# Kernel tuning notes

Measured on AMD Instinct MI355X. Metric: run time of the kernel, lower is better.

## Reference

```python
import jax, jax.numpy as jnp
import numpy as np

EPS = 1e-5
HEADS = 4
DQK = 128
DV = 128
SCALE = DQK ** -0.5


def _bn(x, g, b, m, v):
    # inference-mode BatchNorm over channel dim (axis=1)
    inv = g / jnp.sqrt(v + EPS)
    return x * inv[None, :, None, None] + (b - m * inv)[None, :, None, None]


def setup_inputs() -> dict:
    key = jax.random.key(0)
    ks = jax.random.split(key, 16)
    f = lambda i, shape, s=1.0: jax.random.normal(ks[i], shape, dtype=jnp.float32) * s
    N, Cin, H, W = 16, 2048, 32, 32
    mid = HEADS * DV  # 512
    return {
        "x": f(0, (N, Cin, H, W)),
        "conv1_w": f(1, (mid, Cin), 0.02),
        "gamma1": 1.0 + f(2, (mid,), 0.02),
        "beta1": f(3, (mid,), 0.02),
        "mean1": f(4, (mid,), 0.02),
        "var1": 1.0 + 0.1 * jax.random.uniform(ks[5], (mid,), dtype=jnp.float32),
        "qk_w": f(6, (2 * HEADS * DQK, mid), 0.02),
        "v_w": f(7, (HEADS * DV, mid), 0.02),
        "pos_h": f(8, (H, DQK), SCALE),
        "pos_w": f(9, (W, DQK), SCALE),
        "conv3_w": f(10, (Cin, mid), 0.02),
        "gamma3": 1.0 + f(11, (Cin,), 0.02),
        "beta3": f(12, (Cin,), 0.02),
        "mean3": f(13, (Cin,), 0.02),
        "var3": 1.0 + 0.1 * jax.random.uniform(ks[14], (Cin,), dtype=jnp.float32),
    }


def reference(x, conv1_w, gamma1, beta1, mean1, var1, qk_w, v_w, pos_h, pos_w,
              conv3_w, gamma3, beta3, mean3, var3):
    n, c, h, w = x.shape
    # conv1 (1x1) + BN + ReLU
    out = jnp.einsum('nchw,oc->nohw', x, conv1_w)
    out = jax.nn.relu(_bn(out, gamma1, beta1, mean1, var1))
    # MHSA
    qk = jnp.einsum('nchw,oc->nohw', out, qk_w)  # [n, 2*heads*dqk, h, w]
    vv = jnp.einsum('nchw,oc->nohw', out, v_w)   # [n, heads*dv, h, w]
    q, k = jnp.split(qk, 2, axis=1)

    def to_heads(t):
        d = t.shape[1] // HEADS
        return t.reshape(n, HEADS, d, h * w).transpose(0, 1, 3, 2)  # [n, H, hw, d]

    q, k, vv = to_heads(q), to_heads(k), to_heads(vv)
    q = q * SCALE
    # absolute positional embedding: emb[(h w), d]
    emb = (pos_h[:, None, :] + pos_w[None, :, :]).reshape(h * w, DQK)
    logits = jnp.einsum('nhxd,nhyd->nhxy', q, k) + jnp.einsum('nhxd,yd->nhxy', q, emb)
    weights = jax.nn.softmax(logits, axis=-1)
    attn = jnp.einsum('nhxy,nhyd->nhxd', weights, vv)  # [n, H, hw, dv]
    attn = attn.transpose(0, 1, 3, 2).reshape(n, HEADS * DV, h, w)
    # stride=1 -> avg_pool is identity
    attn = jax.nn.relu(attn)
    # conv3 (1x1) + BN
    out = jnp.einsum('nchw,oc->nohw', attn, conv3_w)
    out = _bn(out, gamma3, beta3, mean3, var3)
    # residual (downsample=None, in==out channels, stride=1) + ReLU
    return jax.nn.relu(out + x)
```

## Files before the change

kernel.cpp:

```cpp
#include <hip/hip_runtime.h>
#include <stdint.h>

typedef __bf16 bf16_t;
typedef __bf16 bf16x8 __attribute__((ext_vector_type(8)));
typedef float f32x4 __attribute__((ext_vector_type(4)));

#define EPSV 1e-5f
#define QSCALE 0.08838834764831845f
#define NB 16
#define HWD 1024
#define CIN 2048
#define MID 512
#define QKLD 1024

__device__ __forceinline__ void gl_lds16(const bf16_t* g, void* l) {
    __builtin_amdgcn_global_load_lds(
        (const __attribute__((address_space(1))) uint32_t*)g,
        (__attribute__((address_space(3))) uint32_t*)l, 16, 0, 0);
}

__device__ __forceinline__ f32x4 mfma16(bf16x8 a, bf16x8 b, f32x4 c) {
    return __builtin_amdgcn_mfma_f32_16x16x32_bf16(a, b, c, 0, 0, 0);
}

#define PW1 (512*2048)
#define PQK (PW1 + 1024*512)
#define PV  (PQK + 512*512)
#define PW3 (PV  + 2048*512)
#define PE  (PW3 + 1024*128)

__global__ void prep_kernel(const float* __restrict__ conv1_w,
                            const float* __restrict__ qk_w,
                            const float* __restrict__ v_w,
                            const float* __restrict__ pos_h,
                            const float* __restrict__ pos_w,
                            const float* __restrict__ conv3_w,
                            bf16_t* __restrict__ w1b, bf16_t* __restrict__ wqkb,
                            bf16_t* __restrict__ wvb, bf16_t* __restrict__ w3b,
                            float* __restrict__ emb) {
    int stride = gridDim.x * blockDim.x;
    for (int i = blockIdx.x * blockDim.x + threadIdx.x; i < PE; i += stride) {
        if (i < PW1) {
            w1b[i] = (bf16_t)conv1_w[i];
        } else if (i < PQK) {
            int j = i - PW1;
            int row = j >> 9;
            float v = (row < 512) ? qk_w[j] * QSCALE : qk_w[j];
            wqkb[j] = (bf16_t)v;
        } else if (i < PV) {
            int j = i - PQK;
            wvb[j] = (bf16_t)v_w[j];
        } else if (i < PW3) {
            int j = i - PV;
            w3b[j] = (bf16_t)conv3_w[j];
        } else {
            int j = i - PW3;
            int y = j >> 7, d = j & 127;
            emb[j] = pos_h[(y >> 5) * 128 + d] + pos_w[(y & 31) * 128 + d];
        }
    }
}

__global__ void transpose_x_kernel(const float* __restrict__ x, bf16_t* __restrict__ xt) {
    __shared__ uint32_t tileT[64][20];
    const int n = blockIdx.z;
    const int c0 = blockIdx.x * 32;
    const int hw0 = blockIdx.y * 64;
    const int t = threadIdx.x;

    const int cp = t >> 4;
    const int hw4 = (t & 15) * 4;
    const float* p0 = x + ((size_t)n * CIN + c0 + 2 * cp) * HWD + hw0 + hw4;
    const float4 a = *(const float4*)p0;
    const float4 b = *(const float4*)(p0 + HWD);
    float av[4] = {a.x, a.y, a.z, a.w};
    float bv[4] = {b.x, b.y, b.z, b.w};
#pragma unroll
    for (int i = 0; i < 4; ++i) {
        uint16_t lo = __builtin_bit_cast(uint16_t, (bf16_t)av[i]);
        uint16_t hi = __builtin_bit_cast(uint16_t, (bf16_t)bv[i]);
        tileT[hw4 + i][cp] = (uint32_t)lo | ((uint32_t)hi << 16);
    }
    __syncthreads();
    const int hw = t >> 2;
    const int seg = (t & 3) * 4;
    uint4 v = *(const uint4*)&tileT[hw][seg];
    *(uint4*)(xt + ((size_t)n * HWD + hw0 + hw) * CIN + c0 + 2 * seg) = v;
}

template <int EPI>
__global__ __launch_bounds__(256, 3)
void gemm_bt(const bf16_t* __restrict__ A, long long aStride,
             const bf16_t* __restrict__ B, long long bStride,
             int K, int ldc,
             const float* __restrict__ e0, const float* __restrict__ e1,
             const float* __restrict__ e2, const float* __restrict__ e3,
             const float* __restrict__ e4, long long e4Stride,
             void* __restrict__ C, long long cStride) {
    __shared__ f32x4 smemv[2048];
    char* smem = (char*)smemv;
    bf16_t* As = (bf16_t*)smem;
    bf16_t* Bs = (bf16_t*)(smem + 16384);
    const int lane = threadIdx.x & 63;
    const int wave = threadIdx.x >> 6;
    const int tN = blockIdx.x * 128, tM = blockIdx.y * 128;
    const int b = blockIdx.z;
    A += (size_t)b * aStride;
    B += (size_t)b * bStride;

    const int wm = (wave >> 1) * 64, wn = (wave & 1) * 64;
    const int lrow = lane & 15, quad = lane >> 4;
    const int srow = lane >> 3;
    const int sgr = lane & 7;
    const int lg = sgr ^ srow;

    f32x4 acc[4][4];
    const f32x4 z4 = {0.f, 0.f, 0.f, 0.f};
#pragma unroll
    for (int i = 0; i < 4; ++i)
#pragma unroll
        for (int j = 0; j < 4; ++j) acc[i][j] = z4;

    for (int k0 = 0; k0 < K; k0 += 64) {
        __syncthreads();
#pragma unroll
        for (int j = 0; j < 4; ++j) {
            const int blk = wave * 4 + j;
            const int row = blk * 8 + srow;
            gl_lds16(A + (size_t)(tM + row) * K + k0 + lg * 8,
                     (char*)As + blk * 1024 + lane * 16);
            gl_lds16(B + (size_t)(tN + row) * K + k0 + lg * 8,
                     (char*)Bs + blk * 1024 + lane * 16);
        }
        __syncthreads();
#pragma unroll
        for (int kh = 0; kh < 2; ++kh) {
            bf16x8 af[4], bfr[4];
#pragma unroll
            for (int t = 0; t < 4; ++t) {
                const int ar = wm + t * 16 + lrow;
                af[t] = *(const bf16x8*)(As + ar * 64 + (((kh * 4 + quad) ^ (ar & 7)) * 8));
                const int br = wn + t * 16 + lrow;
                bfr[t] = *(const bf16x8*)(Bs + br * 64 + (((kh * 4 + quad) ^ (br & 7)) * 8));
            }
#pragma unroll
            for (int i = 0; i < 4; ++i)
#pragma unroll
                for (int j = 0; j < 4; ++j)
                    acc[i][j] = mfma16(af[i], bfr[j], acc[i][j]);
        }
    }

    __syncthreads();
    float* Es = (float*)(smem + wave * 4352);
    const int pr = lane >> 3;
    const int pc = (lane & 7) * 8;
    const int gcol = tN + wn + pc;

#pragma unroll
    for (int i = 0; i < 4; ++i) {
#pragma unroll
        for (int j = 0; j < 4; ++j)
#pragma unroll
            for (int r = 0; r < 4; ++r)
                Es[(quad * 4 + r) * 68 + j * 16 + lrow] = acc[i][j][r];
#pragma unroll
        for (int p = 0; p < 2; ++p) {
            const int lr = p * 8 + pr;
            const int grow = tM + wm + i * 16 + lr;
            float vf[8];
            *(f32x4*)&vf[0] = *(const f32x4*)&Es[lr * 68 + pc];
            *(f32x4*)&vf[4] = *(const f32x4*)&Es[lr * 68 + pc + 4];

            if constexpr (EPI == 1) {
                float gg[8], bt[8], mm[8], vv[8];
                *(f32x4*)&gg[0] = *(const f32x4*)(e0 + gcol);
                *(f32x4*)&gg[4] = *(const f32x4*)(e0 + gcol + 4);
                *(f32x4*)&bt[0] = *(const f32x4*)(e1 + gcol);
                *(f32x4*)&bt[4] = *(const f32x4*)(e1 + gcol + 4);
                *(f32x4*)&mm[0] = *(const f32x4*)(e2 + gcol);
                *(f32x4*)&mm[4] = *(const f32x4*)(e2 + gcol + 4);
                *(f32x4*)&vv[0] = *(const f32x4*)(e3 + gcol);
                *(f32x4*)&vv[4] = *(const f32x4*)(e3 + gcol + 4);
                bf16x8 ob;
#pragma unroll
                for (int c = 0; c < 8; ++c) {
                    float inv = gg[c] * rsqrtf(vv[c] + EPSV);
                    float val = fmaxf(vf[c] * inv + (bt[c] - mm[c] * inv), 0.f);
                    ob[c] = (bf16_t)val;
                }
                bf16_t* Cb = (bf16_t*)C + (size_t)b * cStride;
                *(bf16x8*)(Cb + (size_t)grow * ldc + gcol) = ob;
            } else if constexpr (EPI == 2) {
                bf16x8 ob;
                if (gcol >= 512) {
                    float ev[8];
                    const float* ep = e4 + (size_t)grow * 128 + (gcol & 127);
                    *(f32x4*)&ev[0] = *(const f32x4*)ep;
                    *(f32x4*)&ev[4] = *(const f32x4*)(ep + 4);
#pragma unroll
                    for (int c = 0; c < 8; ++c) ob[c] = (bf16_t)(vf[c] + ev[c]);
                } else {
#pragma unroll
                    for (int c = 0; c < 8; ++c) ob[c] = (bf16_t)vf[c];
                }
                bf16_t* Cb = (bf16_t*)C + (size_t)b * cStride;
                *(bf16x8*)(Cb + (size_t)grow * ldc + gcol) = ob;
            } else if constexpr (EPI == 4) {
                bf16x8 ob;
#pragma unroll
                for (int c = 0; c < 8; ++c) ob[c] = (bf16_t)vf[c];
                bf16_t* Cb = (bf16_t*)C + (size_t)b * cStride;
                *(bf16x8*)(Cb + (size_t)grow * ldc + gcol) = ob;
            } else {
                float g = e0[grow], bet = e1[grow], mn = e2[grow], vr = e3[grow];
                float inv = g * rsqrtf(vr + EPSV);
                float bbv = bet - mn * inv;
                const float* xr = e4 + (size_t)b * e4Stride + (size_t)grow * ldc + gcol;
                f32x4 x0 = *(const f32x4*)xr;
                f32x4 x1 = *(const f32x4*)(xr + 4);
                f32x4 o0, o1;
#pragma unroll
                for (int c = 0; c < 4; ++c) {
                    o0[c] = fmaxf(vf[c] * inv + bbv + x0[c], 0.f);
                    o1[c] = fmaxf(vf[c + 4] * inv + bbv + x1[c], 0.f);
                }
                float* Cf = (float*)C + (size_t)b * cStride + (size_t)grow * ldc + gcol;
                *(f32x4*)Cf = o0;
                *(f32x4*)(Cf + 4) = o1;
            }
        }
    }
}

__global__ __launch_bounds__(256, 2)
void attn_kernel(const bf16_t* __restrict__ qkt, const bf16_t* __restrict__ vt,
                 bf16_t* __restrict__ attn) {
    __shared__ bf16_t Ks[64 * 128];
    __shared__ bf16_t Vs[128 * 64];
    __shared__ bf16_t Ps[4 * 32 * 64];
    const int lane = threadIdx.x & 63;
    const int wave = threadIdx.x >> 6;
    const int qb = blockIdx.x, h = blockIdx.y, n = blockIdx.z;
    const int lrow = lane & 15, quad = lane >> 4;
    const int q0 = qb * 128 + wave * 32;

    bf16x8 qf[2][4];
#pragma unroll
    for (int rt = 0; rt < 2; ++rt)
#pragma unroll
        for (int kf = 0; kf < 4; ++kf)
            qf[rt][kf] = *(const bf16x8*)(qkt + (size_t)(n * HWD + q0 + rt * 16 + lrow) * QKLD
                                          + h * 128 + kf * 32 + quad * 8);

    f32x4 o[2][8];
    const f32x4 z4 = {0.f, 0.f, 0.f, 0.f};
#pragma unroll
    for (int rt = 0; rt < 2; ++rt)
#pragma unroll
        for (int d = 0; d < 8; ++d) o[rt][d] = z4;
    float l[2][4];
#pragma unroll
    for (int rt = 0; rt < 2; ++rt)
#pragma unroll
        for (int r = 0; r < 4; ++r) l[rt][r] = 0.f;

    const bf16_t* kbase = qkt + (size_t)n * HWD * QKLD + 512 + h * 128;
    const bf16_t* vbase = vt + (size_t)((n * 4 + h) * 128) * HWD;

    for (int kc = 0; kc < 16; ++kc) {
        __syncthreads();
#pragma unroll
        for (int j = 0; j < 4; ++j) {
            const int g = wave * 4 + j;
            const int krow = g * 4 + quad;
            const int kgl = lrow ^ (krow & 15);
            gl_lds16(kbase + (size_t)(kc * 64 + krow) * QKLD + kgl * 8,
                     (char*)Ks + g * 1024 + lane * 16);
            const int vrow = g * 8 + (lane >> 3);
            const int vgl = (lane & 7) ^ (vrow & 7);
            gl_lds16(vbase + (size_t)vrow * HWD + kc * 64 + vgl * 8,
                     (char*)Vs + g * 1024 + lane * 16);
        }
        __syncthreads();

        f32x4 s[2][4];
#pragma unroll
        for (int rt = 0; rt < 2; ++rt)
#pragma unroll
            for (int ct = 0; ct < 4; ++ct) s[rt][ct] = z4;
#pragma unroll
        for (int kf = 0; kf < 4; ++kf) {
#pragma unroll
            for (int ct = 0; ct < 4; ++ct) {
                bf16x8 kfrag = *(const bf16x8*)(Ks + (ct * 16 + lrow) * 128
                                                + ((kf * 4 + quad) ^ lrow) * 8);
                s[0][ct] = mfma16(qf[0][kf], kfrag, s[0][ct]);
                s[1][ct] = mfma16(qf[1][kf], kfrag, s[1][ct]);
            }
        }

#pragma unroll
        for (int rt = 0; rt < 2; ++rt) {
#pragma unroll
            for (int r = 0; r < 4; ++r) {
                const int prow = rt * 16 + quad * 4 + r;
                float rs = 0.f;
#pragma unroll
                for (int ct = 0; ct < 4; ++ct) {
                    float p = __expf(s[rt][ct][r]);
                    rs += p;
                    const int pg = (ct * 2 + (lrow >> 3)) ^ (prow & 7);
                    Ps[wave * 2048 + prow * 64 + pg * 8 + (lrow & 7)] = (bf16_t)p;
                }
                l[rt][r] += rs;
            }
        }
        asm volatile("s_waitcnt lgkmcnt(0)" ::: "memory");

#pragma unroll
        for (int kf = 0; kf < 2; ++kf) {
            bf16x8 pa0 = *(const bf16x8*)(Ps + wave * 2048 + lrow * 64
                                          + ((kf * 4 + quad) ^ (lrow & 7)) * 8);
            bf16x8 pa1 = *(const bf16x8*)(Ps + wave * 2048 + (16 + lrow) * 64
                                          + ((kf * 4 + quad) ^ (lrow & 7)) * 8);
#pragma unroll
            for (int d = 0; d < 8; ++d) {
                bf16x8 vf = *(const bf16x8*)(Vs + (d * 16 + lrow) * 64
                                             + ((kf * 4 + quad) ^ (lrow & 7)) * 8);
                o[0][d] = mfma16(pa0, vf, o[0][d]);
                o[1][d] = mfma16(pa1, vf, o[1][d]);
            }
        }
    }

#pragma unroll
    for (int rt = 0; rt < 2; ++rt)
#pragma unroll
        for (int r = 0; r < 4; ++r) {
#pragma unroll
            for (int off = 1; off < 16; off <<= 1)
                l[rt][r] += __shfl_xor(l[rt][r], off, 64);
        }

#pragma unroll
    for (int rt = 0; rt < 2; ++rt) {
#pragma unroll
        for (int r = 0; r < 4; ++r) {
            float linv = 1.f / l[rt][r];
            const size_t row = (size_t)n * HWD + q0 + rt * 16 + quad * 4 + r;
#pragma unroll
            for (int d = 0; d < 8; ++d) {
                float v = o[rt][d][r] * linv;
                v = fmaxf(v, 0.f);
                attn[row * MID + h * 128 + d * 16 + lrow] = (bf16_t)v;
            }
        }
    }
}

extern "C" void kernel_launch(void* const* d_in, const int* in_sizes, int n_in,
                              void* d_out, int out_size, void* d_ws, size_t ws_size,
                              hipStream_t stream) {
    const float* x       = (const float*)d_in[0];
    const float* conv1_w = (const float*)d_in[1];
    const float* gamma1  = (const float*)d_in[2];
    const float* beta1   = (const float*)d_in[3];
    const float* mean1   = (const float*)d_in[4];
    const float* var1    = (const float*)d_in[5];
    const float* qk_w    = (const float*)d_in[6];
    const float* v_w     = (const float*)d_in[7];
    const float* pos_h   = (const float*)d_in[8];
    const float* pos_w   = (const float*)d_in[9];
    const float* conv3_w = (const float*)d_in[10];
    const float* gamma3  = (const float*)d_in[11];
    const float* beta3   = (const float*)d_in[12];
    const float* mean3   = (const float*)d_in[13];
    const float* var3    = (const float*)d_in[14];
    float* out = (float*)d_out;

    char* ws = (char*)d_ws;
    size_t off = 0;
    auto carve = [&](size_t bytes) {
        void* p = ws + off;
        off += (bytes + 255) & ~(size_t)255;
        return p;
    };
    bf16_t* Xt    = (bf16_t*)carve((size_t)NB * HWD * CIN * 2);
    bf16_t* C1t   = (bf16_t*)carve((size_t)NB * HWD * MID * 2);
    bf16_t* QKt   = (bf16_t*)carve((size_t)NB * HWD * QKLD * 2);
    bf16_t* Vt    = (bf16_t*)carve((size_t)NB * 512 * HWD * 2);
    bf16_t* AttnT = (bf16_t*)carve((size_t)NB * HWD * MID * 2);
    bf16_t* W1b   = (bf16_t*)carve((size_t)512 * 2048 * 2);
    bf16_t* Wqkb  = (bf16_t*)carve((size_t)1024 * 512 * 2);
    bf16_t* Wvb   = (bf16_t*)carve((size_t)512 * 512 * 2);
    bf16_t* W3b   = (bf16_t*)carve((size_t)2048 * 512 * 2);
    float*  Emb   = (float*)carve((size_t)1024 * 128 * 4);

    prep_kernel<<<2048, 256, 0, stream>>>(conv1_w, qk_w, v_w, pos_h, pos_w, conv3_w,
                                          W1b, Wqkb, Wvb, W3b, Emb);

    transpose_x_kernel<<<dim3(64, 16, NB), 256, 0, stream>>>(x, Xt);

    gemm_bt<1><<<dim3(4, 8, NB), 256, 0, stream>>>(
        Xt, (long long)HWD * CIN, W1b, 0, CIN, MID,
        gamma1, beta1, mean1, var1, nullptr, 0, C1t, (long long)HWD * MID);

    gemm_bt<2><<<dim3(8, 8, NB), 256, 0, stream>>>(
        C1t, (long long)HWD * MID, Wqkb, 0, MID, QKLD,
        nullptr, nullptr, nullptr, nullptr, Emb, 0, QKt, (long long)HWD * QKLD);

    gemm_bt<4><<<dim3(8, 4, NB), 256, 0, stream>>>(
        Wvb, 0, C1t, (long long)HWD * MID, MID, HWD,
        nullptr, nullptr, nullptr, nullptr, nullptr, 0, Vt, (long long)512 * HWD);

    attn_kernel<<<dim3(8, 4, NB), 256, 0, stream>>>(QKt, Vt, AttnT);

    gemm_bt<3><<<dim3(8, 16, NB), 256, 0, stream>>>(
        W3b, 0, AttnT, (long long)HWD * MID, MID, HWD,
        gamma3, beta3, mean3, var3, x, (long long)CIN * HWD, out, (long long)CIN * HWD);
}
```

Before: 469.6 us.

## Fuse x transpose and bf16 cast into conv1 GEMM A-tile loading

Removes the separate transpose kernel that wrote a bf16 transposed copy of x, and has a new conv1 GEMM kernel read fp32 x directly. It converts x to bf16 and transposes it into swizzled LDS while loading each tile. This avoids writing and re-reading a 64MB intermediate buffer plus one launch. In exchange, A-tile loads become register-staged fp32 loads, four times as many per k-step, instead of async global-to-LDS copies, with no double buffering. The kernel also runs at lower occupancy (launch bounds 2).

```diff
diff --git a/kernel.cpp b/kernel.cpp
--- a/kernel.cpp
+++ b/kernel.cpp
@@ -61,31 +61,120 @@
     }
 }
 
-__global__ void transpose_x_kernel(const float* __restrict__ x, bf16_t* __restrict__ xt) {
-    __shared__ uint32_t tileT[64][20];
-    const int n = blockIdx.z;
-    const int c0 = blockIdx.x * 32;
-    const int hw0 = blockIdx.y * 64;
+__global__ __launch_bounds__(256, 2)
+void gemm1_fused(const float* __restrict__ x,
+                 const bf16_t* __restrict__ B,
+                 const float* __restrict__ e0, const float* __restrict__ e1,
+                 const float* __restrict__ e2, const float* __restrict__ e3,
+                 bf16_t* __restrict__ C) {
+    __shared__ char smem[32768];
+    bf16_t* As = (bf16_t*)smem;
+    bf16_t* Bs = (bf16_t*)(smem + 16384);
     const int t = threadIdx.x;
-
-    const int cp = t >> 4;
-    const int hw4 = (t & 15) * 4;
-    const float* p0 = x + ((size_t)n * CIN + c0 + 2 * cp) * HWD + hw0 + hw4;
-    const float4 a = *(const float4*)p0;
-    const float4 b = *(const float4*)(p0 + HWD);
-    float av[4] = {a.x, a.y, a.z, a.w};
-    float bv[4] = {b.x, b.y, b.z, b.w};
+    const int lane = t & 63;
+    const int wave = t >> 6;
+    const int tN = blockIdx.x * 128, tM = blockIdx.y * 128;
+    const int b = blockIdx.z;
+
+    const int wm = (wave >> 1) * 64, wn = (wave & 1) * 64;
+    const int lrow = lane & 15, quad = lane >> 4;
+    const int srow = lane >> 3;
+    const int sgr = lane & 7;
+    const int lg = sgr ^ srow;
+
+    const int gc = (t >> 5) & 7;
+    const int hwq = (t & 31) * 4;
+
+    f32x4 acc[4][4];
+    const f32x4 z4 = {0.f, 0.f, 0.f, 0.f};
+#pragma unroll
+    for (int i = 0; i < 4; ++i)
+#pragma unroll
+        for (int j = 0; j < 4; ++j) acc[i][j] = z4;
+
+    const float* xb = x + (size_t)b * CIN * HWD + tM + hwq;
+
+    for (int k0 = 0; k0 < CIN; k0 += 64) {
+        __syncthreads();
+#pragma unroll
+        for (int j = 0; j < 4; ++j) {
+            const int blk = wave * 4 + j;
+            const int row = blk * 8 + srow;
+            gl_lds16(B + (size_t)(tN + row) * CIN + k0 + lg * 8,
+                     (char*)Bs + blk * 1024 + lane * 16);
+        }
+        f32x4 xa[8];
+        const float* xp = xb + (size_t)(k0 + gc * 8) * HWD;
+#pragma unroll
+        for (int i = 0; i < 8; ++i) xa[i] = *(const f32x4*)(xp + (size_t)i * HWD);
+#pragma unroll
+        for (int j = 0; j < 4; ++j) {
+            const int ar = hwq + j;
+            const int pg = gc ^ (((ar >> 2) ^ ar) & 7);
+            bf16x8 g;
+#pragma unroll
+            for (int i = 0; i < 8; ++i) g[i] = (bf16_t)xa[i][j];
+            *(bf16x8*)(As + ar * 64 + pg * 8) = g;
+        }
+        __syncthreads();
+#pragma unroll
+        for (int kh = 0; kh < 2; ++kh) {
+            bf16x8 af[4], bfr[4];
+#pragma unroll
+            for (int t4 = 0; t4 < 4; ++t4) {
+                const int ar = wm + t4 * 16 + lrow;
+                const int pga = (kh * 4 + quad) ^ (((ar >> 2) ^ ar) & 7);
+                af[t4] = *(const bf16x8*)(As + ar * 64 + pga * 8);
+                const int br = wn + t4 * 16 + lrow;
+                bfr[t4] = *(const bf16x8*)(Bs + br * 64 + (((kh * 4 + quad) ^ (br & 7)) * 8));
+            }
+#pragma unroll
+            for (int i = 0; i < 4; ++i)
+#pragma unroll
+                for (int j = 0; j < 4; ++j)
+                    acc[i][j] = mfma16(af[i], bfr[j], acc[i][j]);
+        }
+    }
+
+    __syncthreads();
+    float* Es = (float*)(smem + wave * 4352);
+    const int pr = lane >> 3;
+    const int pc = (lane & 7) * 8;
+    const int gcol = tN + wn + pc;
+
 #pragma unroll
     for (int i = 0; i < 4; ++i) {
-        uint16_t lo = __builtin_bit_cast(uint16_t, (bf16_t)av[i]);
-        uint16_t hi = __builtin_bit_cast(uint16_t, (bf16_t)bv[i]);
-        tileT[hw4 + i][cp] = (uint32_t)lo | ((uint32_t)hi << 16);
-    }
-    __syncthreads();
-    const int hw = t >> 2;
-    const int seg = (t & 3) * 4;
-    uint4 v = *(const uint4*)&tileT[hw][seg];
-    *(uint4*)(xt + ((size_t)n * HWD + hw0 + hw) * CIN + c0 + 2 * seg) = v;
+#pragma unroll
+        for (int j = 0; j < 4; ++j)
+#pragma unroll
+            for (int r = 0; r < 4; ++r)
+                Es[(quad * 4 + r) * 68 + j * 16 + lrow] = acc[i][j][r];
+#pragma unroll
+        for (int p = 0; p < 2; ++p) {
+            const int lr = p * 8 + pr;
+            const int grow = tM + wm + i * 16 + lr;
+            float vf[8];
+            *(f32x4*)&vf[0] = *(const f32x4*)&Es[lr * 68 + pc];
+            *(f32x4*)&vf[4] = *(const f32x4*)&Es[lr * 68 + pc + 4];
+            float gg[8], bt[8], mm[8], vv[8];
+            *(f32x4*)&gg[0] = *(const f32x4*)(e0 + gcol);
+            *(f32x4*)&gg[4] = *(const f32x4*)(e0 + gcol + 4);
+            *(f32x4*)&bt[0] = *(const f32x4*)(e1 + gcol);
+            *(f32x4*)&bt[4] = *(const f32x4*)(e1 + gcol + 4);
+            *(f32x4*)&mm[0] = *(const f32x4*)(e2 + gcol);
+            *(f32x4*)&mm[4] = *(const f32x4*)(e2 + gcol + 4);
+            *(f32x4*)&vv[0] = *(const f32x4*)(e3 + gcol);
+            *(f32x4*)&vv[4] = *(const f32x4*)(e3 + gcol + 4);
+            bf16x8 ob;
+#pragma unroll
+            for (int c = 0; c < 8; ++c) {
+                float inv = gg[c] * rsqrtf(vv[c] + EPSV);
+                float val = fmaxf(vf[c] * inv + (bt[c] - mm[c] * inv), 0.f);
+                ob[c] = (bf16_t)val;
+            }
+            *(bf16x8*)(C + (size_t)b * HWD * MID + (size_t)grow * MID + gcol) = ob;
+        }
+    }
 }
 
 template <int EPI>
@@ -172,26 +261,7 @@
             *(f32x4*)&vf[0] = *(const f32x4*)&Es[lr * 68 + pc];
             *(f32x4*)&vf[4] = *(const f32x4*)&Es[lr * 68 + pc + 4];
 
-            if constexpr (EPI == 1) {
-                float gg[8], bt[8], mm[8], vv[8];
-                *(f32x4*)&gg[0] = *(const f32x4*)(e0 + gcol);
-                *(f32x4*)&gg[4] = *(const f32x4*)(e0 + gcol + 4);
-                *(f32x4*)&bt[0] = *(const f32x4*)(e1 + gcol);
-                *(f32x4*)&bt[4] = *(const f32x4*)(e1 + gcol + 4);
-                *(f32x4*)&mm[0] = *(const f32x4*)(e2 + gcol);
-                *(f32x4*)&mm[4] = *(const f32x4*)(e2 + gcol + 4);
-                *(f32x4*)&vv[0] = *(const f32x4*)(e3 + gcol);
-                *(f32x4*)&vv[4] = *(const f32x4*)(e3 + gcol + 4);
-                bf16x8 ob;
-#pragma unroll
-                for (int c = 0; c < 8; ++c) {
-                    float inv = gg[c] * rsqrtf(vv[c] + EPSV);
-                    float val = fmaxf(vf[c] * inv + (bt[c] - mm[c] * inv), 0.f);
-                    ob[c] = (bf16_t)val;
-                }
-                bf16_t* Cb = (bf16_t*)C + (size_t)b * cStride;
-                *(bf16x8*)(Cb + (size_t)grow * ldc + gcol) = ob;
-            } else if constexpr (EPI == 2) {
+            if constexpr (EPI == 2) {
                 bf16x8 ob;
                 if (gcol >= 512) {
                     float ev[8];
@@ -386,7 +456,6 @@
         off += (bytes + 255) & ~(size_t)255;
         return p;
     };
-    bf16_t* Xt    = (bf16_t*)carve((size_t)NB * HWD * CIN * 2);
     bf16_t* C1t   = (bf16_t*)carve((size_t)NB * HWD * MID * 2);
     bf16_t* QKt   = (bf16_t*)carve((size_t)NB * HWD * QKLD * 2);
     bf16_t* Vt    = (bf16_t*)carve((size_t)NB * 512 * HWD * 2);
@@ -400,11 +469,8 @@
     prep_kernel<<<2048, 256, 0, stream>>>(conv1_w, qk_w, v_w, pos_h, pos_w, conv3_w,
                                           W1b, Wqkb, Wvb, W3b, Emb);
 
-    transpose_x_kernel<<<dim3(64, 16, NB), 256, 0, stream>>>(x, Xt);
-
-    gemm_bt<1><<<dim3(4, 8, NB), 256, 0, stream>>>(
-        Xt, (long long)HWD * CIN, W1b, 0, CIN, MID,
-        gamma1, beta1, mean1, var1, nullptr, 0, C1t, (long long)HWD * MID);
+    gemm1_fused<<<dim3(4, 8, NB), 256, 0, stream>>>(
+        x, W1b, gamma1, beta1, mean1, var1, C1t);
 
     gemm_bt<2><<<dim3(8, 8, NB), 256, 0, stream>>>(
         C1t, (long long)HWD * MID, Wqkb, 0, MID, QKLD,
```

Measured after the change: 480.9 us. +2.4%, slower.
